# Performance work log

Measured on AMD Instinct MI355X. Metric: run time of the kernel, lower is better.

The kernel has to match this reference:

```python
import jax, jax.numpy as jnp
import numpy as np

IGNORE_INDEX = -100
LABEL_SMOOTH = 0.1
GAMMA = 2.0
MARGIN = 0.6
SENTENCE_SCALE = 0.1
K = 1000000.0
VOCAB = 32000
B, T = 4, 512


def setup_inputs() -> dict:
    key = jax.random.key(0)
    k1, k2, k3, k4 = jax.random.split(key, 4)
    inp = jax.random.normal(k1, (B, VOCAB, T), dtype=jnp.float32)
    weight = jax.random.uniform(k2, (VOCAB,), dtype=jnp.float32)
    target = jax.random.randint(k3, (B, T), 0, VOCAB, dtype=jnp.int64)
    seq_len = jax.random.randint(k4, (B,), 1, T, dtype=jnp.int64)
    return {"input": inp, "weight": weight, "target": target, "seq_len": seq_len}


def reference(input, weight, target, seq_len):
    V = weight.shape[0]
    b, t = target.shape
    # log-softmax / softmax over vocab dim (axis=1) -- single stable pass
    logp = jax.nn.log_softmax(input, axis=1)          # (B, V, T)
    prob = jnp.exp(logp)                              # == softmax(input, dim=1)
    tgt = target[:, None, :]                          # (B, 1, T)
    # probability of the gold token at each position
    occur_prob = jnp.take_along_axis(prob, tgt, axis=1)[:, 0, :]   # (B, T)
    # predicted token and correctness
    pred = jnp.argmax(input, axis=1)                  # (B, T)
    pred_true = pred == target
    # token occurrence counts (scatter-add) and correct-prediction counts
    flat_tgt = target.reshape(-1)
    all_count = jnp.zeros((V,), jnp.int32).at[flat_tgt].add(1)
    true_count = jnp.zeros((V,), jnp.int32).at[flat_tgt].add(pred_true.reshape(-1).astype(jnp.int32))
    all_count = all_count.at[IGNORE_INDEX].set(0)     # negative index, matches torch
    true_count = true_count.at[IGNORE_INDEX].set(0)
    # label-smoothed cross entropy
    nll = -jnp.take_along_axis(logp, tgt, axis=1)[:, 0, :]          # (B, T)
    false_mean = (-jnp.sum(logp, axis=1) - nll) / (V - 1)           # mean over non-target classes
    ignore_mask = (target != IGNORE_INDEX).astype(logp.dtype)
    loss = (nll * (1.0 - LABEL_SMOOTH) + false_mean * LABEL_SMOOTH) * ignore_mask
    # per-token class weight (max_scale_rate > 0 branch)
    loss = loss * weight[target]
    # focal factor
    loss = loss * (1.0 - occur_prob) ** GAMMA
    # sentence weight (sentence_scale < 1 branch)
    pad = jnp.arange(t)[None, :] >= seq_len[:, None]                # (B, T) padding mask
    sw = jax.nn.sigmoid(K * (MARGIN - occur_prob))
    sw = jnp.where(pad, 0.0, sw).max(axis=1)
    sw = jnp.clip(sw, SENTENCE_SCALE, 1.0)
    loss = loss * sw[:, None]
    return loss, true_count, all_count
```

## Files before the change

### kernel.cpp

```cpp
#include <hip/hip_runtime.h>
#include <math.h>

#define IGNORE_INDEX (-100)
constexpr int Bn   = 4;
constexpr int T    = 512;
constexpr int V    = 32000;
constexpr int COLS = Bn * T;
constexpr int NJ   = 125;
constexpr float LS     = 0.1f;
constexpr float MARGIN = 0.6f;
constexpr float SSCALE = 0.1f;
constexpr float KBIG   = 1000000.0f;

typedef float floatx4 __attribute__((ext_vector_type(4)));

__global__ __launch_bounds__(512, 2) void kA(const float* __restrict__ in,
                                             float4* __restrict__ part,
                                             float* __restrict__ cnt_base) {
    int tid = threadIdx.x;
    int gid = blockIdx.x * 512 + tid;
    if (gid < 2 * V) cnt_base[gid] = 0.f;

    int blk = blockIdx.x;
    int b   = blk / 125;
    int jg  = blk - b * 125;
    int w   = tid >> 6;
    int l   = tid & 63;

    int row0 = jg * 256 + w * 32;
    const float* base = in + ((size_t)b * V + (size_t)row0) * T + (l << 2);

    float m[8], s[8], x[8]; int idx[8];
#pragma unroll
    for (int a = 0; a < 8; ++a) { m[a] = -INFINITY; s[a] = 0.f; x[a] = 0.f; idx[a] = 0; }

    floatx4 bufA[8], bufB[8];

#define LD(BUF, R0)                                                           \
    _Pragma("unroll")                                                         \
    for (int u = 0; u < 4; ++u) {                                             \
        BUF[u*2+0] = *(const floatx4*)(base + (size_t)((R0) + u) * T);        \
        BUF[u*2+1] = *(const floatx4*)(base + (size_t)((R0) + u) * T + 256);  \
    }

#define PR(BUF, R0)                                                           \
    _Pragma("unroll")                                                         \
    for (int u = 0; u < 4; ++u) {                                             \
        int vi = row0 + (R0) + u;                                             \
        _Pragma("unroll")                                                     \
        for (int h = 0; h < 2; ++h) {                                         \
            floatx4 v = BUF[u*2+h];                                           \
            _Pragma("unroll")                                                 \
            for (int k = 0; k < 4; ++k) {                                     \
                int a = h*4 + k;                                              \
                float vv = v[k];                                              \
                s[a] += __expf(vv);                                           \
                if (vv > m[a]) { m[a] = vv; idx[a] = vi; }                    \
                x[a] += vv;                                                   \
            }                                                                 \
        }                                                                     \
    }

    LD(bufA, 0)
    LD(bufB, 4)
    PR(bufA, 0)   LD(bufA, 8)
    PR(bufB, 4)   LD(bufB, 12)
    PR(bufA, 8)   LD(bufA, 16)
    PR(bufB, 12)  LD(bufB, 20)
    PR(bufA, 16)  LD(bufA, 24)
    PR(bufB, 20)  LD(bufB, 28)
    PR(bufA, 24)
    PR(bufB, 28)

#undef LD
#undef PR

    __shared__ float2 smP[8][512];

#pragma unroll
    for (int h = 0; h < 2; ++h)
#pragma unroll
        for (int k = 0; k < 4; ++k) {
            int a = h*4 + k;
            smP[w][h*256 + (l << 2) + k] = make_float2(m[a], __int_as_float(idx[a]));
        }
    __syncthreads();
    float fm, fi;
    {
        float2 v0 = smP[0][tid]; fm = v0.x; fi = v0.y;
#pragma unroll
        for (int q = 1; q < 8; ++q) {
            float2 vq = smP[q][tid];
            if (vq.x > fm) { fm = vq.x; fi = vq.y; }
        }
    }
    __syncthreads();

#pragma unroll
    for (int h = 0; h < 2; ++h)
#pragma unroll
        for (int k = 0; k < 4; ++k) {
            int a = h*4 + k;
            smP[w][h*256 + (l << 2) + k] = make_float2(s[a], x[a]);
        }
    __syncthreads();
    float fs = 0.f, fx = 0.f;
#pragma unroll
    for (int q = 0; q < 8; ++q) {
        float2 vq = smP[q][tid];
        fs += vq.x; fx += vq.y;
    }

    part[(size_t)jg * COLS + b * T + tid] = make_float4(fm, fs, fx, fi);
}

__device__ __forceinline__ float4 merge(float4 a, float4 b) {
    float m = fmaxf(a.x, b.x);
    int idxv = (b.x > a.x) ? __float_as_int(b.w) : __float_as_int(a.w);
    return make_float4(m, a.y + b.y, a.z + b.z, __int_as_float(idxv));
}

__global__ __launch_bounds__(512) void kB(const float4* __restrict__ part,
                                          const float* __restrict__ in,
                                          const float* __restrict__ wgt,
                                          const int*   __restrict__ tgt,
                                          float* __restrict__ loss_base,
                                          float* __restrict__ sig_arr,
                                          float* __restrict__ cnt_true,
                                          float* __restrict__ cnt_all) {
    __shared__ float4 sm[512];
    int tid = threadIdx.x;
    int cl = tid & 31, jg = tid >> 5;
    int c  = blockIdx.x * 32 + cl;

    int tg = 0; float xt = 0.f, wv = 0.f;
    if (tid < 32) {
        int cc = blockIdx.x * 32 + tid;
        tg = tgt[cc];
        int b = cc >> 9, t = cc & 511;
        int tgc = (tg < 0) ? 0 : tg;
        xt = in[((size_t)b * V + (size_t)tgc) * T + t];
        wv = wgt[tgc];
    }

    float4 r = make_float4(-INFINITY, 0.f, 0.f, __int_as_float(0));
#pragma unroll
    for (int jj = 0; jj < 8; ++jj) {
        int j = jg * 8 + jj;
        if (j < NJ) r = merge(r, part[(size_t)j * COLS + c]);
    }
    sm[tid] = r;
    __syncthreads();

    if (tid < 32) {
        float4 r2 = sm[tid];
#pragma unroll
        for (int g = 1; g < 16; ++g) r2 = merge(r2, sm[g * 32 + tid]);

        int cc = blockIdx.x * 32 + tid;
        float sum = r2.y, sumx = r2.z;
        int pred = __float_as_int(r2.w);

        float Z = __logf(sum);
        float xv = (tg == IGNORE_INDEX) ? 0.f : xt;
        float nll = Z - xv;
        float occur = __expf(xv - Z);
        float sum_logp = sumx - (float)V * Z;
        float false_mean = (-sum_logp - nll) / (float)(V - 1);

        float mask = (tg != IGNORE_INDEX) ? 1.f : 0.f;
        float ww = (tg == IGNORE_INDEX) ? 0.f : wv;
        float om = 1.f - occur;
        float loss = (nll * (1.f - LS) + false_mean * LS) * mask * ww * om * om;
        loss_base[cc] = loss;

        if (tg != IGNORE_INDEX) {
            atomicAdd(&cnt_all[tg], 1.0f);
            if (pred == tg) atomicAdd(&cnt_true[tg], 1.0f);
        }

        float z = KBIG * (MARGIN - occur);
        float sig = (z >= 0.f) ? 1.f / (1.f + __expf(-z))
                               : __expf(z) / (1.f + __expf(z));
        sig_arr[cc] = sig;
    }
}

__global__ __launch_bounds__(512) void kC(const float* __restrict__ loss_base,
                                          const float* __restrict__ sig_arr,
                                          const int*   __restrict__ slen,
                                          float* __restrict__ out) {
    __shared__ float red[8];
    int b = blockIdx.x;
    int t = threadIdx.x;
    int c = (b << 9) + t;

    float v = (t < slen[b]) ? sig_arr[c] : 0.f;
#pragma unroll
    for (int off = 32; off > 0; off >>= 1)
        v = fmaxf(v, __shfl_down(v, off, 64));
    if ((t & 63) == 0) red[t >> 6] = v;
    __syncthreads();
    if (t == 0) {
        float m = red[0];
#pragma unroll
        for (int i = 1; i < 8; ++i) m = fmaxf(m, red[i]);
        red[0] = fminf(fmaxf(m, SSCALE), 1.0f);
    }
    __syncthreads();
    float sw = red[0];
    out[c] = loss_base[c] * sw;

    if (b == 0 && t == 0) {
        out[COLS + (V + IGNORE_INDEX)] = 0.f;
        out[COLS + V + (V + IGNORE_INDEX)] = 0.f;
    }
}

extern "C" void kernel_launch(void* const* d_in, const int* in_sizes, int n_in,
                              void* d_out, int out_size, void* d_ws, size_t ws_size,
                              hipStream_t stream) {
    const float* inp  = (const float*)d_in[0];
    const float* wgt  = (const float*)d_in[1];
    const int*   tgt  = (const int*)d_in[2];
    const int*   slen = (const int*)d_in[3];

    float* out = (float*)d_out;
    float* cnt_true = out + COLS;
    float* cnt_all  = out + COLS + V;

    float4* part = (float4*)d_ws;
    float* loss_base = (float*)((char*)d_ws + (size_t)NJ * COLS * sizeof(float4));
    float* sig_arr   = loss_base + COLS;

    kA<<<Bn * NJ, 512, 0, stream>>>(inp, part, cnt_true);
    kB<<<COLS / 32, 512, 0, stream>>>(part, inp, wgt, tgt,
                                      loss_base, sig_arr, cnt_true, cnt_all);
    kC<<<Bn, 512, 0, stream>>>(loss_base, sig_arr, slen, out);
}
```

Baseline: 401.7 us.

## Split vocab reduction into smaller 256-thread blocks with shallower register pipelines

The first-pass kernel now launches 2000 blocks of 256 threads, each covering 64 vocab rows, instead of 500 blocks of 512 threads covering 256 rows. Per-thread double buffering is cut from 8 float4 loads per stage to 2, and launch bounds ask for 8 blocks per CU. The goal is more waves across the CUs and less tail imbalance in the memory-bound log-sum-exp/argmax pass. In exchange, the partial-result buffer grows fourfold, so the merge kernel reads 32 partials per thread group instead of 8. This adds workspace traffic and merge work.

Result: slower. 537.1 us (+33.7%).

```diff
diff --git a/kernel.cpp b/kernel.cpp
--- a/kernel.cpp
+++ b/kernel.cpp
@@ -6,7 +6,7 @@
 constexpr int T    = 512;
 constexpr int V    = 32000;
 constexpr int COLS = Bn * T;
-constexpr int NJ   = 125;
+constexpr int NJ   = 500;
 constexpr float LS     = 0.1f;
 constexpr float MARGIN = 0.6f;
 constexpr float SSCALE = 0.1f;
@@ -14,104 +14,117 @@
 
 typedef float floatx4 __attribute__((ext_vector_type(4)));
 
-__global__ __launch_bounds__(512, 2) void kA(const float* __restrict__ in,
+__global__ __launch_bounds__(256, 8) void kA(const float* __restrict__ in,
                                              float4* __restrict__ part,
                                              float* __restrict__ cnt_base) {
     int tid = threadIdx.x;
-    int gid = blockIdx.x * 512 + tid;
+    int gid = blockIdx.x * 256 + tid;
     if (gid < 2 * V) cnt_base[gid] = 0.f;
 
     int blk = blockIdx.x;
-    int b   = blk / 125;
-    int jg  = blk - b * 125;
+    int b   = blk / 500;
+    int jg  = blk - b * 500;
     int w   = tid >> 6;
     int l   = tid & 63;
 
-    int row0 = jg * 256 + w * 32;
-    const float* base = in + ((size_t)b * V + (size_t)row0) * T + (l << 2);
-
-    float m[8], s[8], x[8]; int idx[8];
-#pragma unroll
-    for (int a = 0; a < 8; ++a) { m[a] = -INFINITY; s[a] = 0.f; x[a] = 0.f; idx[a] = 0; }
-
-    floatx4 bufA[8], bufB[8];
-
-#define LD(BUF, R0)                                                           \
-    _Pragma("unroll")                                                         \
-    for (int u = 0; u < 4; ++u) {                                             \
-        BUF[u*2+0] = *(const floatx4*)(base + (size_t)((R0) + u) * T);        \
-        BUF[u*2+1] = *(const floatx4*)(base + (size_t)((R0) + u) * T + 256);  \
-    }
-
-#define PR(BUF, R0)                                                           \
-    _Pragma("unroll")                                                         \
-    for (int u = 0; u < 4; ++u) {                                             \
-        int vi = row0 + (R0) + u;                                             \
-        _Pragma("unroll")                                                     \
-        for (int h = 0; h < 2; ++h) {                                         \
-            floatx4 v = BUF[u*2+h];                                           \
-            _Pragma("unroll")                                                 \
-            for (int k = 0; k < 4; ++k) {                                     \
-                int a = h*4 + k;                                              \
-                float vv = v[k];                                              \
-                s[a] += __expf(vv);                                           \
-                if (vv > m[a]) { m[a] = vv; idx[a] = vi; }                    \
-                x[a] += vv;                                                   \
-            }                                                                 \
-        }                                                                     \
-    }
-
-    LD(bufA, 0)
-    LD(bufB, 4)
-    PR(bufA, 0)   LD(bufA, 8)
-    PR(bufB, 4)   LD(bufB, 12)
-    PR(bufA, 8)   LD(bufA, 16)
-    PR(bufB, 12)  LD(bufB, 20)
-    PR(bufA, 16)  LD(bufA, 24)
-    PR(bufB, 20)  LD(bufB, 28)
-    PR(bufA, 24)
-    PR(bufB, 28)
-
-#undef LD
-#undef PR
-
-    __shared__ float2 smP[8][512];
-
-#pragma unroll
-    for (int h = 0; h < 2; ++h)
-#pragma unroll
-        for (int k = 0; k < 4; ++k) {
-            int a = h*4 + k;
-            smP[w][h*256 + (l << 2) + k] = make_float2(m[a], __int_as_float(idx[a]));
+    int row0 = jg * 64 + w * 16;
+    const float* rb = in + ((size_t)b * V + (size_t)row0) * T + (l << 2);
+
+    float m0=-INFINITY,m1=-INFINITY,m2=-INFINITY,m3=-INFINITY;
+    float m4=-INFINITY,m5=-INFINITY,m6=-INFINITY,m7=-INFINITY;
+    float s0=0,s1=0,s2=0,s3=0,s4=0,s5=0,s6=0,s7=0;
+    float x0=0,x1=0,x2=0,x3=0,x4=0,x5=0,x6=0,x7=0;
+    int   i0=0,i1=0,i2=0,i3=0,i4=0,i5=0,i6=0,i7=0;
+
+    floatx4 a0, c0, a1, c1;
+
+#define ROWL(P, Q, R) {                                                      \
+    P = *(const floatx4*)(rb + (size_t)(R) * T);                             \
+    Q = *(const floatx4*)(rb + (size_t)(R) * T + 256); }
+
+#define ROWP(P, Q, R) {                                                      \
+    int vi = row0 + (R); float e;                                            \
+    e=(P).x; s0+=__expf(e); if(e>m0){m0=e;i0=vi;} x0+=e;                     \
+    e=(P).y; s1+=__expf(e); if(e>m1){m1=e;i1=vi;} x1+=e;                     \
+    e=(P).z; s2+=__expf(e); if(e>m2){m2=e;i2=vi;} x2+=e;                     \
+    e=(P).w; s3+=__expf(e); if(e>m3){m3=e;i3=vi;} x3+=e;                     \
+    e=(Q).x; s4+=__expf(e); if(e>m4){m4=e;i4=vi;} x4+=e;                     \
+    e=(Q).y; s5+=__expf(e); if(e>m5){m5=e;i5=vi;} x5+=e;                     \
+    e=(Q).z; s6+=__expf(e); if(e>m6){m6=e;i6=vi;} x6+=e;                     \
+    e=(Q).w; s7+=__expf(e); if(e>m7){m7=e;i7=vi;} x7+=e; }
+
+    ROWL(a0, c0, 0)  ROWL(a1, c1, 1)
+    ROWP(a0, c0, 0)  ROWL(a0, c0, 2)
+    ROWP(a1, c1, 1)  ROWL(a1, c1, 3)
+    ROWP(a0, c0, 2)  ROWL(a0, c0, 4)
+    ROWP(a1, c1, 3)  ROWL(a1, c1, 5)
+    ROWP(a0, c0, 4)  ROWL(a0, c0, 6)
+    ROWP(a1, c1, 5)  ROWL(a1, c1, 7)
+    ROWP(a0, c0, 6)  ROWL(a0, c0, 8)
+    ROWP(a1, c1, 7)  ROWL(a1, c1, 9)
+    ROWP(a0, c0, 8)  ROWL(a0, c0, 10)
+    ROWP(a1, c1, 9)  ROWL(a1, c1, 11)
+    ROWP(a0, c0, 10) ROWL(a0, c0, 12)
+    ROWP(a1, c1, 11) ROWL(a1, c1, 13)
+    ROWP(a0, c0, 12) ROWL(a0, c0, 14)
+    ROWP(a1, c1, 13) ROWL(a1, c1, 15)
+    ROWP(a0, c0, 14)
+    ROWP(a1, c1, 15)
+
+#undef ROWL
+#undef ROWP
+
+    __shared__ float2 smP[4][512];
+
+    {
+        int c4 = l << 2;
+        smP[w][c4+0]     = make_float2(m0, __int_as_float(i0));
+        smP[w][c4+1]     = make_float2(m1, __int_as_float(i1));
+        smP[w][c4+2]     = make_float2(m2, __int_as_float(i2));
+        smP[w][c4+3]     = make_float2(m3, __int_as_float(i3));
+        smP[w][256+c4+0] = make_float2(m4, __int_as_float(i4));
+        smP[w][256+c4+1] = make_float2(m5, __int_as_float(i5));
+        smP[w][256+c4+2] = make_float2(m6, __int_as_float(i6));
+        smP[w][256+c4+3] = make_float2(m7, __int_as_float(i7));
+    }
+    __syncthreads();
+    float fmA, fiA, fmB, fiB;
+    {
+        float2 vA = smP[0][tid];       fmA = vA.x; fiA = vA.y;
+        float2 vB = smP[0][tid + 256]; fmB = vB.x; fiB = vB.y;
+#pragma unroll
+        for (int q = 1; q < 4; ++q) {
+            float2 qA = smP[q][tid];
+            float2 qB = smP[q][tid + 256];
+            if (qA.x > fmA) { fmA = qA.x; fiA = qA.y; }
+            if (qB.x > fmB) { fmB = qB.x; fiB = qB.y; }
         }
-    __syncthreads();
-    float fm, fi;
+    }
+    __syncthreads();
+
     {
-        float2 v0 = smP[0][tid]; fm = v0.x; fi = v0.y;
-#pragma unroll
-        for (int q = 1; q < 8; ++q) {
-            float2 vq = smP[q][tid];
-            if (vq.x > fm) { fm = vq.x; fi = vq.y; }
-        }
-    }
-    __syncthreads();
-
-#pragma unroll
-    for (int h = 0; h < 2; ++h)
-#pragma unroll
-        for (int k = 0; k < 4; ++k) {
-            int a = h*4 + k;
-            smP[w][h*256 + (l << 2) + k] = make_float2(s[a], x[a]);
-        }
-    __syncthreads();
-    float fs = 0.f, fx = 0.f;
-#pragma unroll
-    for (int q = 0; q < 8; ++q) {
-        float2 vq = smP[q][tid];
-        fs += vq.x; fx += vq.y;
-    }
-
-    part[(size_t)jg * COLS + b * T + tid] = make_float4(fm, fs, fx, fi);
+        int c4 = l << 2;
+        smP[w][c4+0]     = make_float2(s0, x0);
+        smP[w][c4+1]     = make_float2(s1, x1);
+        smP[w][c4+2]     = make_float2(s2, x2);
+        smP[w][c4+3]     = make_float2(s3, x3);
+        smP[w][256+c4+0] = make_float2(s4, x4);
+        smP[w][256+c4+1] = make_float2(s5, x5);
+        smP[w][256+c4+2] = make_float2(s6, x6);
+        smP[w][256+c4+3] = make_float2(s7, x7);
+    }
+    __syncthreads();
+    float fsA = 0.f, fxA = 0.f, fsB = 0.f, fxB = 0.f;
+#pragma unroll
+    for (int q = 0; q < 4; ++q) {
+        float2 qA = smP[q][tid];
+        float2 qB = smP[q][tid + 256];
+        fsA += qA.x; fxA += qA.y;
+        fsB += qB.x; fxB += qB.y;
+    }
+
+    part[(size_t)jg * COLS + b * T + tid]       = make_float4(fmA, fsA, fxA, fiA);
+    part[(size_t)jg * COLS + b * T + tid + 256] = make_float4(fmB, fsB, fxB, fiB);
 }
 
 __device__ __forceinline__ float4 merge(float4 a, float4 b) {
@@ -144,9 +157,9 @@
     }
 
     float4 r = make_float4(-INFINITY, 0.f, 0.f, __int_as_float(0));
-#pragma unroll
-    for (int jj = 0; jj < 8; ++jj) {
-        int j = jg * 8 + jj;
+#pragma unroll 8
+    for (int jj = 0; jj < 32; ++jj) {
+        int j = jg * 32 + jj;
         if (j < NJ) r = merge(r, part[(size_t)j * COLS + c]);
     }
     sm[tid] = r;
@@ -233,7 +246,7 @@
     float* loss_base = (float*)((char*)d_ws + (size_t)NJ * COLS * sizeof(float4));
     float* sig_arr   = loss_base + COLS;
 
-    kA<<<Bn * NJ, 512, 0, stream>>>(inp, part, cnt_true);
+    kA<<<Bn * NJ, 256, 0, stream>>>(inp, part, cnt_true);
     kB<<<COLS / 32, 512, 0, stream>>>(part, inp, wgt, tgt,
                                       loss_base, sig_arr, cnt_true, cnt_all);
     kC<<<Bn, 512, 0, stream>>>(loss_base, sig_arr, slen, out);
```
